# Performance work log

Hardware: AMD Instinct MI355X
Metric: run time of the kernel (lower is better)

The kernel has to match this reference:

```python
import jax, jax.numpy as jnp
import numpy as np

N, E, F, HID, HEADS, NCLS, NGRAPH = 50000, 800000, 116, 32, 4, 2, 100

def _glorot(key, shape):
    fan_in, fan_out = shape[0], shape[-1]
    lim = jnp.sqrt(6.0 / (fan_in + fan_out))
    return jax.random.uniform(key, shape, jnp.float32, -lim, lim)

def setup_inputs() -> dict:
    key = jax.random.key(0)
    ks = jax.random.split(key, 20)
    in1 = F + HID                 # node feats concat edge_msg
    in2 = HID * HEADS             # conv1 output (concat heads)
    return {
        "x": jax.random.normal(ks[0], (N, F), jnp.float32),
        "edge_attr": jax.random.uniform(ks[1], (E,), jnp.float32),
        "edge_index": jax.random.randint(ks[2], (2, E), 0, N, jnp.int32),
        "batch": jnp.sort(jax.random.randint(ks[3], (N,), 0, NGRAPH, jnp.int32)),
        "We": _glorot(ks[4], (1, HID)),   "be": jnp.zeros((HID,), jnp.float32),
        "W1l": _glorot(ks[5], (in1, HEADS * HID)), "b1l": jnp.zeros((HEADS * HID,), jnp.float32),
        "W1r": _glorot(ks[6], (in1, HEADS * HID)), "b1r": jnp.zeros((HEADS * HID,), jnp.float32),
        "att1": _glorot(ks[7], (HEADS, HID)).reshape(1, HEADS, HID),
        "bias1": jnp.zeros((HEADS * HID,), jnp.float32),
        "W2l": _glorot(ks[8], (in2, HID)), "b2l": jnp.zeros((HID,), jnp.float32),
        "W2r": _glorot(ks[9], (in2, HID)), "b2r": jnp.zeros((HID,), jnp.float32),
        "att2": _glorot(ks[10], (1, HID)).reshape(1, 1, HID),
        "bias2": jnp.zeros((HID,), jnp.float32),
        "Wfc": _glorot(ks[11], (HID, NCLS)), "bfc": jnp.zeros((NCLS,), jnp.float32),
    }

def _gatv2_conv(x, src, dst, Wl, bl, Wr, br, att, bias, heads, ch):
    # PyG GATv2Conv, eval mode (attention dropout off), negative_slope=0.2
    n = x.shape[0]
    xl = (x @ Wl + bl).reshape(n, heads, ch)          # source transform
    xr = (x @ Wr + br).reshape(n, heads, ch)          # target transform
    xj = xl[src]                                       # [E,H,C] gathered source
    e = jnp.sum(att * jax.nn.leaky_relu(xj + xr[dst], 0.2), axis=-1)  # [E,H]
    emax = jax.ops.segment_max(e, dst, num_segments=n)
    ez = jnp.exp(e - emax[dst])
    denom = jax.ops.segment_sum(ez, dst, num_segments=n)
    alpha = ez / (denom[dst] + 1e-16)                  # segment softmax over targets
    out = jax.ops.segment_sum(alpha[..., None] * xj, dst, num_segments=n)  # [N,H,C]
    return out.reshape(n, heads * ch) + bias

def reference(x, edge_attr, edge_index, batch, We, be, W1l, b1l, W1r, b1r, att1, bias1,
              W2l, b2l, W2r, b2r, att2, bias2, Wfc, bfc):
    n = x.shape[0]
    src0, dst0 = edge_index[0], edge_index[1]
    # edge feature aggregation: Linear(1,hid) then index_add onto target nodes
    edge_feat = edge_attr[:, None] @ We + be           # [E,HID]
    edge_msg = jax.ops.segment_sum(edge_feat, dst0, num_segments=n)
    h = jnp.concatenate([x, edge_msg], axis=1)         # [N, F+HID]
    # GATv2Conv adds self-loops by default
    loop = jnp.arange(n, dtype=edge_index.dtype)
    src = jnp.concatenate([src0, loop])
    dst = jnp.concatenate([dst0, loop])
    h = _gatv2_conv(h, src, dst, W1l, b1l, W1r, b1r, att1, bias1, HEADS, HID)
    h = jax.nn.elu(h)                                  # dropout is identity in eval
    h = _gatv2_conv(h, src, dst, W2l, b2l, W2r, b2r, att2, bias2, 1, HID)
    h = jax.nn.elu(h)
    # global mean pool over graphs
    sums = jax.ops.segment_sum(h, batch, num_segments=NGRAPH)
    cnt = jax.ops.segment_sum(jnp.ones((n,), h.dtype), batch, num_segments=NGRAPH)
    pooled = sums / jnp.maximum(cnt, 1.0)[:, None]
    logits = pooled @ Wfc + bfc
    return jax.nn.log_softmax(logits, axis=1)
```

## Files before the change

### kernel.cpp

```cpp
#include <hip/hip_runtime.h>
#include <hip/hip_bf16.h>
#include <math.h>

#define N_NODES 50000
#define N_EDGES 800000
#define F_IN    116
#define HID     32
#define HEADS   4
#define NGRAPH  100
#define IN1     (F_IN + HID)
#define IN2     (HID * HEADS)

#define EXP_SHIFT_MUL  1.44269504f
#define EXP_SHIFT_SUB  43.2808512f

typedef __attribute__((ext_vector_type(8))) short bf16x8;
typedef __attribute__((ext_vector_type(4))) float f32x4;

__device__ inline unsigned pack_bf2(float a, float b) {
    unsigned lo = __bfloat16_as_ushort(__float2bfloat16(a));
    unsigned hi = __bfloat16_as_ushort(__float2bfloat16(b));
    return lo | (hi << 16);
}

__global__ void k_count(const int* __restrict__ ei, const float* __restrict__ attr,
                        int* __restrict__ cnt, float* __restrict__ ssum, int E) {
    int e = blockIdx.x * blockDim.x + threadIdx.x;
    if (e >= E) return;
    int d = ei[E + e];
    atomicAdd(&cnt[d], 1);
    atomicAdd(&ssum[d], attr[e]);
}

__global__ __launch_bounds__(1024)
void k_scan(const int* __restrict__ cnt, int* __restrict__ offs, int n) {
    __shared__ int lds[1024];
    int t = threadIdx.x;
    int chunk = (n + 1023) / 1024;
    int base = t * chunk;
    int lim = min(base + chunk, n);
    int local = 0;
    for (int i = base; i < lim; ++i) local += cnt[i];
    lds[t] = local;
    __syncthreads();
    for (int off = 1; off < 1024; off <<= 1) {
        int v = (t >= off) ? lds[t - off] : 0;
        __syncthreads();
        lds[t] += v;
        __syncthreads();
    }
    int run = lds[t] - local;
    for (int i = base; i < lim; ++i) { offs[i] = run; run += cnt[i]; }
}

__global__ void k_fill(const int* __restrict__ ei, int* __restrict__ offs,
                       int* __restrict__ csr, int E) {
    int e = blockIdx.x * blockDim.x + threadIdx.x;
    if (e >= E) return;
    int d = ei[E + e];
    int pos = atomicAdd(&offs[d], 1);
    csr[pos] = ei[e];
}

#define KPAD1 168
__global__ __launch_bounds__(256)
void k_mm1(const float* __restrict__ x, const float* __restrict__ ssum,
           const int* __restrict__ cnt, const float* __restrict__ We,
           const float* __restrict__ be, const float* __restrict__ W,
           const float* __restrict__ bias, unsigned short* __restrict__ Cb, int M) {
    __shared__ short As[64][KPAD1];
    __shared__ short Ws[128][KPAD1];
    int tid = threadIdx.x;
    int rowBase = blockIdx.x * 64;
    {
        int r = tid >> 2;
        int p0 = tid & 3;
        int row = rowBase + r;
        bool rv = row < M;
        float ss = rv ? ssum[row] : 0.f;
        float cf = rv ? (float)cnt[row] : 0.f;
        const float* xrp = x + (size_t)row * F_IN;
#pragma unroll
        for (int i = 0; i < 21; ++i) {
            int p = p0 + i * 4;
            int k = 2 * p;
            float v0 = 0.f, v1 = 0.f;
            if (rv && k < IN1) {
                if (k < F_IN) {
                    float2 t = *(const float2*)(xrp + k);
                    v0 = t.x; v1 = t.y;
                } else {
                    int j = k - F_IN;
                    v0 = We[j] * ss + be[j] * cf;
                    v1 = We[j + 1] * ss + be[j + 1] * cf;
                }
            }
            ((int*)&As[r][0])[p] = (int)pack_bf2(v0, v1);
        }
    }
    {
        int c = tid & 127;
        int ph = tid >> 7;
#pragma unroll
        for (int i = 0; i < 42; ++i) {
            int p = ph + 2 * i;
            int k = 2 * p;
            float v0 = (k < IN1) ? W[k * 128 + c] : 0.f;
            float v1 = (k + 1 < IN1) ? W[(k + 1) * 128 + c] : 0.f;
            ((int*)&Ws[c][0])[p] = (int)pack_bf2(v0, v1);
        }
    }
    __syncthreads();

    int wid = tid >> 6, l = tid & 63;
    int wm = wid >> 1, wn = wid & 1;
    int mBase = wm * 32, nBase = wn * 64;
    int lr = l & 15, lg = l >> 4;
    f32x4 acc[2][4] = {};
#pragma unroll
    for (int ks = 0; ks < 5; ++ks) {
        int k0 = ks * 32 + lg * 8;
        bf16x8 a0 = *(bf16x8*)&As[mBase + lr][k0];
        bf16x8 a1 = *(bf16x8*)&As[mBase + 16 + lr][k0];
        bf16x8 b0 = *(bf16x8*)&Ws[nBase + lr][k0];
        bf16x8 b1 = *(bf16x8*)&Ws[nBase + 16 + lr][k0];
        bf16x8 b2 = *(bf16x8*)&Ws[nBase + 32 + lr][k0];
        bf16x8 b3 = *(bf16x8*)&Ws[nBase + 48 + lr][k0];
        acc[0][0] = __builtin_amdgcn_mfma_f32_16x16x32_bf16(a0, b0, acc[0][0], 0, 0, 0);
        acc[0][1] = __builtin_amdgcn_mfma_f32_16x16x32_bf16(a0, b1, acc[0][1], 0, 0, 0);
        acc[0][2] = __builtin_amdgcn_mfma_f32_16x16x32_bf16(a0, b2, acc[0][2], 0, 0, 0);
        acc[0][3] = __builtin_amdgcn_mfma_f32_16x16x32_bf16(a0, b3, acc[0][3], 0, 0, 0);
        acc[1][0] = __builtin_amdgcn_mfma_f32_16x16x32_bf16(a1, b0, acc[1][0], 0, 0, 0);
        acc[1][1] = __builtin_amdgcn_mfma_f32_16x16x32_bf16(a1, b1, acc[1][1], 0, 0, 0);
        acc[1][2] = __builtin_amdgcn_mfma_f32_16x16x32_bf16(a1, b2, acc[1][2], 0, 0, 0);
        acc[1][3] = __builtin_amdgcn_mfma_f32_16x16x32_bf16(a1, b3, acc[1][3], 0, 0, 0);
    }
#pragma unroll
    for (int mf = 0; mf < 2; ++mf)
#pragma unroll
        for (int nf = 0; nf < 4; ++nf) {
            int col = nBase + nf * 16 + lr;
            float bs = bias[col];
#pragma unroll
            for (int r = 0; r < 4; ++r) {
                int row = rowBase + mBase + mf * 16 + lg * 4 + r;
                if (row < M)
                    Cb[(size_t)row * 128 + col] =
                        __bfloat16_as_ushort(__float2bfloat16(acc[mf][nf][r] + bs));
            }
        }
}

#define KPAD2 136
__global__ __launch_bounds__(256)
void k_mm2(const unsigned* __restrict__ h1, const float* __restrict__ Wl,
           const float* __restrict__ bl, const float* __restrict__ Wr,
           const float* __restrict__ br, float* __restrict__ xl2,
           float* __restrict__ xr2, int M) {
    __shared__ short As[64][KPAD2];
    __shared__ short Ws[64][KPAD2];
    int tid = threadIdx.x;
    int rowBase = blockIdx.x * 64;
    {
        int r = tid >> 2;
        int s0 = tid & 3;
        int row = rowBase + r;
        bool rv = row < M;
#pragma unroll
        for (int i = 0; i < 17; ++i) {
            int slot = s0 + 4 * i;
            unsigned u = (rv && slot < 64) ? h1[(size_t)row * 64 + slot] : 0u;
            ((int*)&As[r][0])[slot] = (int)u;
        }
    }
    {
        int c = tid & 63;
        int ph = tid >> 6;
#pragma unroll
        for (int i = 0; i < 17; ++i) {
            int p = ph + 4 * i;
            int k = 2 * p;
            float v0 = 0.f, v1 = 0.f;
            if (k < IN2) {
                if (c < 32) { v0 = Wl[k * 32 + c]; v1 = Wl[(k + 1) * 32 + c]; }
                else        { v0 = Wr[k * 32 + c - 32]; v1 = Wr[(k + 1) * 32 + c - 32]; }
            }
            ((int*)&Ws[c][0])[p] = (int)pack_bf2(v0, v1);
        }
    }
    __syncthreads();

    int wid = tid >> 6, l = tid & 63;
    int wm = wid >> 1, wn = wid & 1;
    int mBase = wm * 32, nBase = wn * 32;
    int lr = l & 15, lg = l >> 4;
    f32x4 acc[2][2] = {};
#pragma unroll
    for (int ks = 0; ks < 4; ++ks) {
        int k0 = ks * 32 + lg * 8;
        bf16x8 a0 = *(bf16x8*)&As[mBase + lr][k0];
        bf16x8 a1 = *(bf16x8*)&As[mBase + 16 + lr][k0];
        bf16x8 b0 = *(bf16x8*)&Ws[nBase + lr][k0];
        bf16x8 b1 = *(bf16x8*)&Ws[nBase + 16 + lr][k0];
        acc[0][0] = __builtin_amdgcn_mfma_f32_16x16x32_bf16(a0, b0, acc[0][0], 0, 0, 0);
        acc[0][1] = __builtin_amdgcn_mfma_f32_16x16x32_bf16(a0, b1, acc[0][1], 0, 0, 0);
        acc[1][0] = __builtin_amdgcn_mfma_f32_16x16x32_bf16(a1, b0, acc[1][0], 0, 0, 0);
        acc[1][1] = __builtin_amdgcn_mfma_f32_16x16x32_bf16(a1, b1, acc[1][1], 0, 0, 0);
    }
#pragma unroll
    for (int mf = 0; mf < 2; ++mf)
#pragma unroll
        for (int nf = 0; nf < 2; ++nf) {
            int cg = nBase + nf * 16 + lr;
#pragma unroll
            for (int r = 0; r < 4; ++r) {
                int row = rowBase + mBase + mf * 16 + lg * 4 + r;
                if (row < M) {
                    float v = acc[mf][nf][r];
                    if (cg < 32) xl2[(size_t)row * 32 + cg] = v + bl[cg];
                    else         xr2[(size_t)row * 32 + cg - 32] = v + br[cg - 32];
                }
            }
        }
}

__global__ __launch_bounds__(256)
void k_conv1(const unsigned* __restrict__ xl, const unsigned* __restrict__ xr,
             const int* __restrict__ csr, const int* __restrict__ offs_end,
             const int* __restrict__ cnt, const float* __restrict__ att,
             const float* __restrict__ bias, unsigned* __restrict__ h1, int n_nodes) {
    int wave = threadIdx.x >> 6;
    int lane = threadIdx.x & 63;
    int half = lane >> 5;
    int l32 = lane & 31;
    int n = blockIdx.x * 4 + wave;
    if (n >= n_nodes) return;
    int c_n = cnt[n];
    int start = offs_end[n] - c_n;
    int total = c_n + 1;

    uint2 urv = *(const uint2*)(xr + (size_t)n * 64 + 2 * l32);
    float xr0 = __uint_as_float(urv.x << 16);
    float xr1 = __uint_as_float(urv.x & 0xffff0000u);
    float xr2v = __uint_as_float(urv.y << 16);
    float xr3 = __uint_as_float(urv.y & 0xffff0000u);
    float4 av = *(const float4*)(att + 4 * l32);

    int tmax = (total + 1) >> 1;
    int item0 = half;
    bool v_cur = item0 < total;
    int src_cur = (item0 == 0 || !v_cur) ? n : csr[start];
    uint2 u_cur = *(const uint2*)(xl + (size_t)src_cur * 64 + 2 * l32);
    int item1 = 2 + half;
    bool v_n = item1 < total;
    int src_n = v_n ? csr[start + item1 - 1] : n;

    float s = 0.f, a0 = 0.f, a1 = 0.f, a2 = 0.f, a3 = 0.f;
    for (int t = 0; t < tmax; ++t) {
        uint2 u_next = *(const uint2*)(xl + (size_t)src_n * 64 + 2 * l32);
        int item2 = 2 * (t + 2) + half;
        bool v_n2 = item2 < total;
        int src_n2 = v_n2 ? csr[start + item2 - 1] : n;

        float x0 = __uint_as_float(u_cur.x << 16);
        float x1 = __uint_as_float(u_cur.x & 0xffff0000u);
        float x2 = __uint_as_float(u_cur.y << 16);
        float x3 = __uint_as_float(u_cur.y & 0xffff0000u);
        float t0 = x0 + xr0, t1 = x1 + xr1, t2 = x2 + xr2v, t3 = x3 + xr3;
        float p = av.x * (fmaxf(t0, 0.f) + 0.2f * fminf(t0, 0.f))
                + av.y * (fmaxf(t1, 0.f) + 0.2f * fminf(t1, 0.f))
                + av.z * (fmaxf(t2, 0.f) + 0.2f * fminf(t2, 0.f))
                + av.w * (fmaxf(t3, 0.f) + 0.2f * fminf(t3, 0.f));
        p += __shfl_xor(p, 1);
        p += __shfl_xor(p, 2);
        p += __shfl_xor(p, 4);
        float ez = v_cur ? exp2f(p * EXP_SHIFT_MUL - EXP_SHIFT_SUB) : 0.f;
        s += ez;
        a0 += ez * x0; a1 += ez * x1; a2 += ez * x2; a3 += ez * x3;

        u_cur = u_next; v_cur = v_n; v_n = v_n2; src_n = src_n2;
    }
    s  += __shfl_xor(s, 32);
    a0 += __shfl_xor(a0, 32);
    a1 += __shfl_xor(a1, 32);
    a2 += __shfl_xor(a2, 32);
    a3 += __shfl_xor(a3, 32);
    if (half == 0) {
        float inv = 1.f / s;
        float4 bv = *(const float4*)(bias + 4 * l32);
        float o0 = a0 * inv + bv.x;
        float o1 = a1 * inv + bv.y;
        float o2 = a2 * inv + bv.z;
        float o3 = a3 * inv + bv.w;
        o0 = o0 > 0.f ? o0 : __expf(o0) - 1.f;
        o1 = o1 > 0.f ? o1 : __expf(o1) - 1.f;
        o2 = o2 > 0.f ? o2 : __expf(o2) - 1.f;
        o3 = o3 > 0.f ? o3 : __expf(o3) - 1.f;
        uint2 w;
        w.x = pack_bf2(o0, o1);
        w.y = pack_bf2(o2, o3);
        *(uint2*)(h1 + (size_t)n * 64 + 2 * l32) = w;
    }
}

__global__ __launch_bounds__(256)
void k_conv2(const float* __restrict__ xl, const float* __restrict__ xr,
             const int* __restrict__ csr, const int* __restrict__ offs_end,
             const int* __restrict__ cnt, const float* __restrict__ att,
             const float* __restrict__ bias, float* __restrict__ out, int n_nodes) {
    int wave = threadIdx.x >> 6;
    int lane = threadIdx.x & 63;
    int half = lane >> 5;
    int c = lane & 31;
    int n = blockIdx.x * 8 + wave * 2 + half;
    bool nvalid = n < n_nodes;
    int nn = nvalid ? n : 0;
    int c_n = nvalid ? cnt[nn] : -1;
    int start = offs_end[nn] - max(c_n, 0);
    int total = c_n + 1;
    int t_other = __shfl_xor(total, 32);
    int tmax = max(total, t_other);
    float xr_v = xr[(size_t)nn * 32 + c];
    float att_v = att[c];
    float xj_cur = xl[(size_t)nn * 32 + c];
    int src_n = (1 < total) ? csr[start] : nn;
    float s = 0.f, acc = 0.f;
    for (int j = 0; j < tmax; ++j) {
        float xj_next = xl[(size_t)src_n * 32 + c];
        int jn2 = j + 2;
        int src_n2 = (jn2 < total && jn2 > 0) ? csr[start + jn2 - 1] : nn;
        bool valid = j < total;
        float t = xj_cur + xr_v;
        float lk = fmaxf(t, 0.f) + 0.2f * fminf(t, 0.f);
        float p = att_v * lk;
#pragma unroll
        for (int mk = 16; mk >= 1; mk >>= 1) p += __shfl_xor(p, mk);
        float ez = valid ? exp2f(p * EXP_SHIFT_MUL - EXP_SHIFT_SUB) : 0.f;
        s += ez;
        acc += ez * xj_cur;
        xj_cur = xj_next; src_n = src_n2;
    }
    if (nvalid) {
        float o = acc / s + bias[c];
        out[(size_t)nn * 32 + c] = o > 0.f ? o : __expf(o) - 1.f;
    }
}

__global__ __launch_bounds__(256)
void k_pool(const float* __restrict__ h2, const int* __restrict__ batch,
            float* __restrict__ pooled, float* __restrict__ gcnt, int n_nodes) {
    __shared__ float lp[NGRAPH * HID];
    __shared__ float lc[NGRAPH];
    for (int i = threadIdx.x; i < NGRAPH * HID; i += 256) lp[i] = 0.f;
    for (int i = threadIdx.x; i < NGRAPH; i += 256) lc[i] = 0.f;
    __syncthreads();
    int totalElems = n_nodes * HID;
    int per = (totalElems + gridDim.x - 1) / gridDim.x;
    int s0 = blockIdx.x * per;
    int s1 = min(s0 + per, totalElems);
    for (int i = s0 + threadIdx.x; i < s1; i += 256) {
        int n = i >> 5, cc = i & 31;
        int g = batch[n];
        atomicAdd(&lp[g * HID + cc], h2[i]);
        if (cc == 0) atomicAdd(&lc[g], 1.f);
    }
    __syncthreads();
    for (int i = threadIdx.x; i < NGRAPH * HID; i += 256)
        if (lp[i] != 0.f) atomicAdd(&pooled[i], lp[i]);
    for (int i = threadIdx.x; i < NGRAPH; i += 256)
        if (lc[i] != 0.f) atomicAdd(&gcnt[i], lc[i]);
}

__global__ void k_final(const float* __restrict__ pooled, const float* __restrict__ gcnt,
                        const float* __restrict__ Wfc, const float* __restrict__ bfc,
                        float* __restrict__ out) {
    int g = blockIdx.x * blockDim.x + threadIdx.x;
    if (g >= NGRAPH) return;
    float inv = 1.f / fmaxf(gcnt[g], 1.f);
    float z0 = bfc[0], z1 = bfc[1];
    for (int c = 0; c < HID; ++c) {
        float mv = pooled[g * HID + c] * inv;
        z0 += mv * Wfc[c * 2 + 0];
        z1 += mv * Wfc[c * 2 + 1];
    }
    float mx = fmaxf(z0, z1);
    float lse = mx + logf(expf(z0 - mx) + expf(z1 - mx));
    out[g * 2 + 0] = z0 - lse;
    out[g * 2 + 1] = z1 - lse;
}

extern "C" void kernel_launch(void* const* d_in, const int* in_sizes, int n_in,
                              void* d_out, int out_size, void* d_ws, size_t ws_size,
                              hipStream_t stream) {
    const float* x     = (const float*)d_in[0];
    const float* eattr = (const float*)d_in[1];
    const int*   eidx  = (const int*)d_in[2];
    const int*   batch = (const int*)d_in[3];
    const float* We    = (const float*)d_in[4];
    const float* be    = (const float*)d_in[5];
    const float* W1l   = (const float*)d_in[6];
    const float* b1l   = (const float*)d_in[7];
    const float* W1r   = (const float*)d_in[8];
    const float* b1r   = (const float*)d_in[9];
    const float* att1  = (const float*)d_in[10];
    const float* bias1 = (const float*)d_in[11];
    const float* W2l   = (const float*)d_in[12];
    const float* b2l   = (const float*)d_in[13];
    const float* W2r   = (const float*)d_in[14];
    const float* b2r   = (const float*)d_in[15];
    const float* att2  = (const float*)d_in[16];
    const float* bias2 = (const float*)d_in[17];
    const float* Wfc   = (const float*)d_in[18];
    const float* bfc   = (const float*)d_in[19];
    float* out = (float*)d_out;

    char* ws = (char*)d_ws;
    size_t off = 0;
    auto alloc = [&](size_t bytes) {
        void* p = ws + off;
        off += (bytes + 255) & ~size_t(255);
        return p;
    };
    int*      cnt    = (int*)     alloc(N_NODES * 4);
    int*      offs   = (int*)     alloc(N_NODES * 4);
    float*    ssum   = (float*)   alloc(N_NODES * 4);
    int*      csr    = (int*)     alloc(N_EDGES * 4);
    unsigned* xl1    = (unsigned*)alloc((size_t)N_NODES * 64 * 4);
    unsigned* xr1    = (unsigned*)alloc((size_t)N_NODES * 64 * 4);
    unsigned* h1     = (unsigned*)alloc((size_t)N_NODES * 64 * 4);
    float*    pooled = (float*)   alloc(NGRAPH * HID * 4);
    float*    gcnt   = (float*)   alloc(NGRAPH * 4);
    float* xl2 = (float*)xl1;
    float* xr2 = xl2 + (size_t)N_NODES * 32;
    float* h2  = xr2 + (size_t)N_NODES * 32;

    hipMemsetAsync(cnt, 0, N_NODES * 4, stream);
    hipMemsetAsync(ssum, 0, N_NODES * 4, stream);
    hipMemsetAsync(pooled, 0, NGRAPH * HID * 4, stream);
    hipMemsetAsync(gcnt, 0, NGRAPH * 4, stream);

    int ebl = (N_EDGES + 255) / 256;
    k_count<<<ebl, 256, 0, stream>>>(eidx, eattr, cnt, ssum, N_EDGES);
    k_scan<<<1, 1024, 0, stream>>>(cnt, offs, N_NODES);
    k_fill<<<ebl, 256, 0, stream>>>(eidx, offs, csr, N_EDGES);

    int gbl = (N_NODES + 63) / 64;
    k_mm1<<<gbl, 256, 0, stream>>>(x, ssum, cnt, We, be, W1l, b1l,
                                   (unsigned short*)xl1, N_NODES);
    k_mm1<<<gbl, 256, 0, stream>>>(x, ssum, cnt, We, be, W1r, b1r,
                                   (unsigned short*)xr1, N_NODES);

    k_conv1<<<(N_NODES + 3) / 4, 256, 0, stream>>>(
        xl1, xr1, csr, offs, cnt, att1, bias1, h1, N_NODES);

    k_mm2<<<gbl, 256, 0, stream>>>(h1, W2l, b2l, W2r, b2r, xl2, xr2, N_NODES);

    k_conv2<<<(N_NODES + 7) / 8, 256, 0, stream>>>(
        xl2, xr2, csr, offs, cnt, att2, bias2, h2, N_NODES);

    k_pool<<<256, 256, 0, stream>>>(h2, batch, pooled, gcnt, N_NODES);
    k_final<<<1, 128, 0, stream>>>(pooled, gcnt, Wfc, bfc, out);
}
```

Baseline: 474.2 us.

## Replace single-block prefix scan with three-phase multi-block scan, merge memsets

The single 1024-thread block scan, in which each thread walked about 49 consecutive counts serially, is replaced by a reduce-then-scan-then-propagate scheme spread over about 196 blocks. This is meant to remove a serial, one-CU bottleneck on the CSR build path. The workspace is also rearranged so that cnt and ssum are contiguous, and pooled and gcnt likewise, which cuts four memsets to two. The cost is two extra kernel launches.

```diff
diff --git a/kernel.cpp b/kernel.cpp
--- a/kernel.cpp
+++ b/kernel.cpp
@@ -10,6 +10,7 @@
 #define NGRAPH  100
 #define IN1     (F_IN + HID)
 #define IN2     (HID * HEADS)
+#define NB_SCAN ((N_NODES + 255) / 256)
 
 #define EXP_SHIFT_MUL  1.44269504f
 #define EXP_SHIFT_SUB  43.2808512f
@@ -32,25 +33,56 @@
     atomicAdd(&ssum[d], attr[e]);
 }
 
-__global__ __launch_bounds__(1024)
-void k_scan(const int* __restrict__ cnt, int* __restrict__ offs, int n) {
-    __shared__ int lds[1024];
+__global__ __launch_bounds__(256)
+void k_scan_a(const int* __restrict__ cnt, int* __restrict__ bsum, int n) {
+    __shared__ int lds[256];
     int t = threadIdx.x;
-    int chunk = (n + 1023) / 1024;
-    int base = t * chunk;
-    int lim = min(base + chunk, n);
-    int local = 0;
-    for (int i = base; i < lim; ++i) local += cnt[i];
-    lds[t] = local;
-    __syncthreads();
-    for (int off = 1; off < 1024; off <<= 1) {
-        int v = (t >= off) ? lds[t - off] : 0;
+    int i = blockIdx.x * 256 + t;
+    int v = (i < n) ? cnt[i] : 0;
+    lds[t] = v;
+    __syncthreads();
+#pragma unroll
+    for (int off = 128; off >= 1; off >>= 1) {
+        if (t < off) lds[t] += lds[t + off];
         __syncthreads();
-        lds[t] += v;
+    }
+    if (t == 0) bsum[blockIdx.x] = lds[0];
+}
+
+__global__ __launch_bounds__(256)
+void k_scan_b(int* __restrict__ bsum, int* __restrict__ boff) {
+    __shared__ int lds[256];
+    int t = threadIdx.x;
+    int v = (t < NB_SCAN) ? bsum[t] : 0;
+    lds[t] = v;
+    __syncthreads();
+#pragma unroll
+    for (int off = 1; off < 256; off <<= 1) {
+        int u = (t >= off) ? lds[t - off] : 0;
         __syncthreads();
-    }
-    int run = lds[t] - local;
-    for (int i = base; i < lim; ++i) { offs[i] = run; run += cnt[i]; }
+        lds[t] += u;
+        __syncthreads();
+    }
+    if (t < NB_SCAN) boff[t] = lds[t] - v;
+}
+
+__global__ __launch_bounds__(256)
+void k_scan_c(const int* __restrict__ cnt, const int* __restrict__ boff,
+              int* __restrict__ offs, int n) {
+    __shared__ int lds[256];
+    int t = threadIdx.x;
+    int i = blockIdx.x * 256 + t;
+    int v = (i < n) ? cnt[i] : 0;
+    lds[t] = v;
+    __syncthreads();
+#pragma unroll
+    for (int off = 1; off < 256; off <<= 1) {
+        int u = (t >= off) ? lds[t - off] : 0;
+        __syncthreads();
+        lds[t] += u;
+        __syncthreads();
+    }
+    if (i < n) offs[i] = boff[blockIdx.x] + lds[t] - v;
 }
 
 __global__ void k_fill(const int* __restrict__ ei, int* __restrict__ offs,
@@ -422,26 +454,28 @@
         return p;
     };
     int*      cnt    = (int*)     alloc(N_NODES * 4);
+    float*    ssum   = (float*)   alloc(N_NODES * 4);
     int*      offs   = (int*)     alloc(N_NODES * 4);
-    float*    ssum   = (float*)   alloc(N_NODES * 4);
+    int*      bsum   = (int*)     alloc(NB_SCAN * 4);
+    int*      boff   = (int*)     alloc(NB_SCAN * 4);
     int*      csr    = (int*)     alloc(N_EDGES * 4);
     unsigned* xl1    = (unsigned*)alloc((size_t)N_NODES * 64 * 4);
     unsigned* xr1    = (unsigned*)alloc((size_t)N_NODES * 64 * 4);
     unsigned* h1     = (unsigned*)alloc((size_t)N_NODES * 64 * 4);
-    float*    pooled = (float*)   alloc(NGRAPH * HID * 4);
-    float*    gcnt   = (float*)   alloc(NGRAPH * 4);
+    float*    pooled = (float*)   alloc(NGRAPH * (HID + 1) * 4);
+    float*    gcnt   = pooled + NGRAPH * HID;
     float* xl2 = (float*)xl1;
     float* xr2 = xl2 + (size_t)N_NODES * 32;
     float* h2  = xr2 + (size_t)N_NODES * 32;
 
-    hipMemsetAsync(cnt, 0, N_NODES * 4, stream);
-    hipMemsetAsync(ssum, 0, N_NODES * 4, stream);
-    hipMemsetAsync(pooled, 0, NGRAPH * HID * 4, stream);
-    hipMemsetAsync(gcnt, 0, NGRAPH * 4, stream);
+    hipMemsetAsync(cnt, 0, 2 * N_NODES * 4 + 256, stream);
+    hipMemsetAsync(pooled, 0, NGRAPH * (HID + 1) * 4, stream);
 
     int ebl = (N_EDGES + 255) / 256;
     k_count<<<ebl, 256, 0, stream>>>(eidx, eattr, cnt, ssum, N_EDGES);
-    k_scan<<<1, 1024, 0, stream>>>(cnt, offs, N_NODES);
+    k_scan_a<<<NB_SCAN, 256, 0, stream>>>(cnt, bsum, N_NODES);
+    k_scan_b<<<1, 256, 0, stream>>>(bsum, boff);
+    k_scan_c<<<NB_SCAN, 256, 0, stream>>>(cnt, boff, offs, N_NODES);
     k_fill<<<ebl, 256, 0, stream>>>(eidx, offs, csr, N_EDGES);
 
     int gbl = (N_NODES + 63) / 64;
```

Result: faster. 402.9 us (-15.1%).
